# Kernel tuning notes

Hardware: AMD Instinct MI355X
Metric: run time of the kernel (lower is better)

## Reference

```python
import jax, jax.numpy as jnp
import numpy as np

B = 256
NUM_CAPS = 2            # digit capsules
N_IN = 6 * 6 * 6 * 32   # 6912 input capsules
D_OUT = 16
D_IN = 8
N_ROUTING = 3           # original loops range(3 - 1) = 2 iterations
EPS = 1e-9


def squash(s):
    # squash along last axis: (|s|^2/(1+|s|^2)) * s/|s|
    n2 = jnp.sum(s * s, axis=-1, keepdims=True)
    return (n2 / (1.0 + n2)) * s / jnp.sqrt(n2 + EPS)


def setup_inputs() -> dict:
    key = jax.random.key(0)
    k1, k2 = jax.random.split(key)
    x = jax.random.normal(k1, (B, N_IN, D_IN), dtype=jnp.float32)
    W = jax.random.normal(k2, (NUM_CAPS, N_IN, D_OUT, D_IN), dtype=jnp.float32) * 0.1
    return {"x": x, "W": W}


def reference(x, W):
    # tile x over the 2 digit capsules + per-(capsule, input-capsule) matvec:
    # u_hat[b,j,n,e] = sum_d W[j,n,e,d] * x[b,n,d]   -> [B, 2, N, 16]
    u_hat = jnp.einsum('bnd,jned->bjne', x, W)
    b_logits = jnp.zeros(u_hat.shape[:3], dtype=x.dtype)  # [B, 2, N]
    v = None
    for _ in range(N_ROUTING - 1):
        c = jax.nn.softmax(b_logits, axis=1)               # softmax over the 2 capsules (dim=1 in source)
        s = jnp.einsum('bjn,bjne->bje', c, u_hat)          # [B, 2, 16]
        v = squash(s)
        b_logits = b_logits + jnp.einsum('bje,bjne->bjn', v, u_hat)
    return v
```

## Files before the change

kernel.cpp:

```cpp
#include <hip/hip_runtime.h>

#define B_ 256
#define J_ 2
#define N_ 6912
#define E_ 16
#define D_ 8
#define NBT 18
#define CGX 384
#define TOT4 (J_*NBT*32)
#define BSTR (4*N_*D_)

__device__ __forceinline__ float dpp_row_add16(float v){
  v += __int_as_float(__builtin_amdgcn_update_dpp(0, __float_as_int(v), 0xB1,  0xF, 0xF, true));
  v += __int_as_float(__builtin_amdgcn_update_dpp(0, __float_as_int(v), 0x4E,  0xF, 0xF, true));
  v += __int_as_float(__builtin_amdgcn_update_dpp(0, __float_as_int(v), 0x141, 0xF, 0xF, true));
  v += __int_as_float(__builtin_amdgcn_update_dpp(0, __float_as_int(v), 0x140, 0xF, 0xF, true));
  return v;
}

__device__ __forceinline__ void ldx(const float* __restrict__ xp, int ni,
                                    float4 (&xa)[4], float4 (&xb)[4]){
  #pragma unroll
  for (int k=0;k<4;++k){
    xa[k] = *(const float4*)(xp + (size_t)k*BSTR + ni*8);
    xb[k] = *(const float4*)(xp + (size_t)k*BSTR + ni*8 + 4);
  }
}

__device__ __forceinline__ void body1(const float4* __restrict__ smem4, int ni,
                                      int sA, int sB,
                                      const float4 (&xa)[4], const float4 (&xb)[4],
                                      float (&acc0)[4], float (&acc1)[4]){
  const float4 wa0 = smem4[ni*32 + sA];
  const float4 wb0 = smem4[ni*32 + sB];
  const float4 wa1 = smem4[(NBT + ni)*32 + sA];
  const float4 wb1 = smem4[(NBT + ni)*32 + sB];
  #pragma unroll
  for (int k=0;k<4;++k){
    float a0 = acc0[k], a1 = acc1[k];
    a0 = fmaf(wa0.x, xa[k].x, a0); a0 = fmaf(wa0.y, xa[k].y, a0);
    a0 = fmaf(wa0.z, xa[k].z, a0); a0 = fmaf(wa0.w, xa[k].w, a0);
    a0 = fmaf(wb0.x, xb[k].x, a0); a0 = fmaf(wb0.y, xb[k].y, a0);
    a0 = fmaf(wb0.z, xb[k].z, a0); a0 = fmaf(wb0.w, xb[k].w, a0);
    a1 = fmaf(wa1.x, xa[k].x, a1); a1 = fmaf(wa1.y, xa[k].y, a1);
    a1 = fmaf(wa1.z, xa[k].z, a1); a1 = fmaf(wa1.w, xa[k].w, a1);
    a1 = fmaf(wb1.x, xb[k].x, a1); a1 = fmaf(wb1.y, xb[k].y, a1);
    a1 = fmaf(wb1.z, xb[k].z, a1); a1 = fmaf(wb1.w, xb[k].w, a1);
    acc0[k] = a0; acc1[k] = a1;
  }
}

__device__ __forceinline__ void body2(const float4* __restrict__ smem4, int ni,
                                      int sA, int sB,
                                      const float4 (&xa)[4], const float4 (&xb)[4],
                                      const float (&vj0)[4], const float (&vj1)[4],
                                      float (&acc0)[4], float (&acc1)[4]){
  const float4 wa0 = smem4[ni*32 + sA];
  const float4 wb0 = smem4[ni*32 + sB];
  const float4 wa1 = smem4[(NBT + ni)*32 + sA];
  const float4 wb1 = smem4[(NBT + ni)*32 + sB];
  float u0[4], u1[4];
  #pragma unroll
  for (int k=0;k<4;++k){
    float a0, a1;
    a0 = wa0.x*xa[k].x;            a0 = fmaf(wa0.y, xa[k].y, a0);
    a0 = fmaf(wa0.z, xa[k].z, a0); a0 = fmaf(wa0.w, xa[k].w, a0);
    a0 = fmaf(wb0.x, xb[k].x, a0); a0 = fmaf(wb0.y, xb[k].y, a0);
    a0 = fmaf(wb0.z, xb[k].z, a0); a0 = fmaf(wb0.w, xb[k].w, a0);
    a1 = wa1.x*xa[k].x;            a1 = fmaf(wa1.y, xa[k].y, a1);
    a1 = fmaf(wa1.z, xa[k].z, a1); a1 = fmaf(wa1.w, xa[k].w, a1);
    a1 = fmaf(wb1.x, xb[k].x, a1); a1 = fmaf(wb1.y, xb[k].y, a1);
    a1 = fmaf(wb1.z, xb[k].z, a1); a1 = fmaf(wb1.w, xb[k].w, a1);
    u0[k] = a0; u1[k] = a1;
  }
  #pragma unroll
  for (int k=0;k<4;++k){
    const float d  = dpp_row_add16(fmaf(vj1[k], u1[k], -(vj0[k]*u0[k])));
    const float c0 = __builtin_amdgcn_rcpf(1.f + __expf(d));
    acc0[k] = fmaf(c0,       u0[k], acc0[k]);
    acc1[k] = fmaf(1.f - c0, u1[k], acc1[k]);
  }
}

__device__ __forceinline__ void stageW(const float* __restrict__ W, int nb0, int tid,
                                       float* __restrict__ smem){
  {
    float4 buf[3];
    #pragma unroll
    for (int k=0;k<3;++k){
      const int idx = k*256 + tid;
      const int j  = (idx >= NBT*32) ? 1 : 0;
      const int r4 = idx - j*(NBT*32);
      buf[k] = *(const float4*)(W + ((size_t)j*N_ + nb0)*(E_*D_) + (size_t)r4*4);
    }
    #pragma unroll
    for (int k=0;k<3;++k){
      const int idx = k*256 + tid;
      const int u = idx & 31;
      *(float4*)(smem + (size_t)((idx & ~31) | (u ^ (u>>3)))*4) = buf[k];
    }
  }
  {
    float4 buf[2];
    #pragma unroll
    for (int k=0;k<2;++k){
      const int idx = (k+3)*256 + tid;
      if (idx < TOT4){
        const int j  = (idx >= NBT*32) ? 1 : 0;
        const int r4 = idx - j*(NBT*32);
        buf[k] = *(const float4*)(W + ((size_t)j*N_ + nb0)*(E_*D_) + (size_t)r4*4);
      }
    }
    #pragma unroll
    for (int k=0;k<2;++k){
      const int idx = (k+3)*256 + tid;
      if (idx < TOT4){
        const int u = idx & 31;
        *(float4*)(smem + (size_t)((idx & ~31) | (u ^ (u>>3)))*4) = buf[k];
      }
    }
  }
}


__global__ __launch_bounds__(256, 4) void kpass1(const float* __restrict__ x,
                                                 const float* __restrict__ W,
                                                 float* __restrict__ partial)
{
  __shared__ float smem[TOT4*4];
  const int tid  = threadIdx.x;
  const int lane = tid & 63;
  const int wv   = __builtin_amdgcn_readfirstlane(tid >> 6);
  const int e    = lane & 15;
  const int blo  = lane >> 4;
  const int nb0  = blockIdx.x * NBT;
  const int b0   = blockIdx.y*64 + wv*16 + blo;
  const float* xp = x + ((size_t)b0*N_ + nb0)*D_;
  const int sA = (e*2)   ^ ((e*2)>>3);
  const int sB = (e*2+1) ^ ((e*2+1)>>3);
  const float4* smem4 = (const float4*)smem;

  stageW(W, nb0, tid, smem);
  float4 xaA[4], xbA[4], xaB[4], xbB[4];
  ldx(xp, 0, xaA, xbA);
  __syncthreads();

  float acc0[4] = {0,0,0,0}, acc1[4] = {0,0,0,0};
  #pragma unroll 1
  for (int ni=0; ni<NBT; ni+=2){
    ldx(xp, ni+1, xaB, xbB);
    body1(smem4, ni,   sA, sB, xaA, xbA, acc0, acc1);
    if (ni+2 < NBT) ldx(xp, ni+2, xaA, xbA);
    body1(smem4, ni+1, sA, sB, xaB, xbB, acc0, acc1);
  }

  float* dst = partial + (size_t)(blockIdx.x*4 + blockIdx.y)*2048
             + (wv*16 + blo)*32 + e;
  #pragma unroll
  for (int k=0;k<4;++k){ dst[k*128] = acc0[k]; dst[k*128+16] = acc1[k]; }
}

__global__ __launch_bounds__(256, 4) void kpass2(const float* __restrict__ x,
                                                 const float* __restrict__ W,
                                                 const float* __restrict__ v1,
                                                 float* __restrict__ partial)
{
  __shared__ float smem[TOT4*4];
  const int tid  = threadIdx.x;
  const int lane = tid & 63;
  const int wv   = __builtin_amdgcn_readfirstlane(tid >> 6);
  const int e    = lane & 15;
  const int blo  = lane >> 4;
  const int nb0  = blockIdx.x * NBT;
  const int b0   = blockIdx.y*64 + wv*16 + blo;
  const float* xp = x + ((size_t)b0*N_ + nb0)*D_;
  const int sA = (e*2)   ^ ((e*2)>>3);
  const int sB = (e*2+1) ^ ((e*2+1)>>3);
  const float4* smem4 = (const float4*)smem;

  stageW(W, nb0, tid, smem);
  float4 xaA[4], xbA[4], xaB[4], xbB[4];
  ldx(xp, 0, xaA, xbA);
  float vj0[4], vj1[4];
  #pragma unroll
  for (int k=0;k<4;++k){
    vj0[k] = v1[(size_t)(b0 + 4*k)*32 + e];
    vj1[k] = v1[(size_t)(b0 + 4*k)*32 + 16 + e];
  }
  __syncthreads();

  float acc0[4] = {0,0,0,0}, acc1[4] = {0,0,0,0};
  #pragma unroll 1
  for (int ni=0; ni<NBT; ni+=2){
    ldx(xp, ni+1, xaB, xbB);
    body2(smem4, ni,   sA, sB, xaA, xbA, vj0, vj1, acc0, acc1);
    if (ni+2 < NBT) ldx(xp, ni+2, xaA, xbA);
    body2(smem4, ni+1, sA, sB, xaB, xbB, vj0, vj1, acc0, acc1);
  }

  float* dst = partial + (size_t)(blockIdx.x*4 + blockIdx.y)*2048
             + (wv*16 + blo)*32 + e;
  #pragma unroll
  for (int k=0;k<4;++k){ dst[k*128] = acc0[k]; dst[k*128+16] = acc1[k]; }
}

template<bool HALF>
__global__ __launch_bounds__(256) void kred(const float* __restrict__ partial,
                                            float* __restrict__ dst)
{
  __shared__ float sh[128];
  const int tid  = threadIdx.x;
  const int o    = blockIdx.x*128 + (tid & 127);
  const int half = tid >> 7;
  const int btile = o >> 11, q = o & 2047;
  const float* p = partial + (size_t)btile*2048 + q + (size_t)half*(CGX/2)*8192;
  float s = 0.f;
  #pragma unroll 24
  for (int cx=0; cx<CGX/2; ++cx) s += p[(size_t)cx*8192];
  if (half) sh[tid & 127] = s;
  __syncthreads();
  if (!half){
    s += sh[tid & 127];
    if (HALF) s *= 0.5f;
    float n2 = s*s;
    #pragma unroll
    for (int m=1; m<16; m<<=1) n2 += __shfl_xor(n2, m);
    dst[o] = s * (n2/(1.f+n2)) * rsqrtf(n2 + 1e-9f);
  }
}

#define NT 512
__global__ __launch_bounds__(NT) void kmono(const float* __restrict__ x,
                                            const float* __restrict__ W,
                                            float* __restrict__ out)
{
  const int b    = blockIdx.x;
  const int tid  = threadIdx.x;
  const int wv   = tid >> 6;
  const int lane = tid & 63;
  __shared__ float wred[8*33];
  __shared__ float vsh[32];

  float acc[32];
  #pragma unroll
  for (int i=0;i<32;++i) acc[i]=0.f;
  for (int n = tid; n < N_; n += NT){
    const float4 xa = *(const float4*)(x + ((size_t)b*N_ + n)*D_);
    const float4 xb = *(const float4*)(x + ((size_t)b*N_ + n)*D_ + 4);
    #pragma unroll
    for (int j=0;j<J_;++j){
      const float* wp = W + ((size_t)j*N_ + n)*(E_*D_);
      #pragma unroll
      for (int e=0;e<E_;++e){
        const float4 wa = *(const float4*)(wp + e*8);
        const float4 wb = *(const float4*)(wp + e*8 + 4);
        float a = acc[j*16+e];
        a = fmaf(wa.x,xa.x,a); a = fmaf(wa.y,xa.y,a); a = fmaf(wa.z,xa.z,a); a = fmaf(wa.w,xa.w,a);
        a = fmaf(wb.x,xb.x,a); a = fmaf(wb.y,xb.y,a); a = fmaf(wb.z,xb.z,a); a = fmaf(wb.w,xb.w,a);
        acc[j*16+e] = a;
      }
    }
  }
  #pragma unroll
  for (int i=0;i<32;++i){
    float v = acc[i];
    #pragma unroll
    for (int off=32; off; off>>=1) v += __shfl_xor(v, off);
    acc[i] = v;
  }
  if (lane == 0){
    #pragma unroll
    for (int i=0;i<32;++i) wred[wv*33 + i] = acc[i];
  }
  __syncthreads();
  if (tid < 32){
    float s = 0.f;
    #pragma unroll
    for (int w=0;w<8;++w) s += wred[w*33 + tid];
    wred[tid] = 0.5f * s;
  }
  __syncthreads();
  if (tid < 32){
    const int j = tid >> 4; float n2 = 0.f;
    #pragma unroll
    for (int e=0;e<16;++e){ const float sv = wred[j*16+e]; n2 = fmaf(sv,sv,n2); }
    vsh[tid] = wred[tid] * (n2/(1.f+n2)) * rsqrtf(n2 + 1e-9f);
  }
  __syncthreads();
  float vv[32];
  #pragma unroll
  for (int i=0;i<32;++i) vv[i] = vsh[i];

  #pragma unroll
  for (int i=0;i<32;++i) acc[i]=0.f;
  for (int n = tid; n < N_; n += NT){
    const float4 xa = *(const float4*)(x + ((size_t)b*N_ + n)*D_);
    const float4 xb = *(const float4*)(x + ((size_t)b*N_ + n)*D_ + 4);
    float u[32];
    #pragma unroll
    for (int j=0;j<J_;++j){
      const float* wp = W + ((size_t)j*N_ + n)*(E_*D_);
      #pragma unroll
      for (int e=0;e<E_;++e){
        const float4 wa = *(const float4*)(wp + e*8);
        const float4 wb = *(const float4*)(wp + e*8 + 4);
        float a;
        a = wa.x*xa.x; a = fmaf(wa.y,xa.y,a); a = fmaf(wa.z,xa.z,a); a = fmaf(wa.w,xa.w,a);
        a = fmaf(wb.x,xb.x,a); a = fmaf(wb.y,xb.y,a); a = fmaf(wb.z,xb.z,a); a = fmaf(wb.w,xb.w,a);
        u[j*16+e] = a;
      }
    }
    float l0=0.f, l1=0.f;
    #pragma unroll
    for (int e=0;e<16;++e){ l0 = fmaf(vv[e],u[e],l0); l1 = fmaf(vv[16+e],u[16+e],l1); }
    const float c0 = 1.f/(1.f + __expf(l1 - l0));
    const float c1 = 1.f - c0;
    #pragma unroll
    for (int e=0;e<16;++e){ acc[e] = fmaf(c0,u[e],acc[e]); acc[16+e] = fmaf(c1,u[16+e],acc[16+e]); }
  }
  #pragma unroll
  for (int i=0;i<32;++i){
    float v = acc[i];
    #pragma unroll
    for (int off=32; off; off>>=1) v += __shfl_xor(v, off);
    acc[i] = v;
  }
  __syncthreads();
  if (lane == 0){
    #pragma unroll
    for (int i=0;i<32;++i) wred[wv*33 + i] = acc[i];
  }
  __syncthreads();
  if (tid < 32){
    float s = 0.f;
    #pragma unroll
    for (int w=0;w<8;++w) s += wred[w*33 + tid];
    wred[tid] = s;
  }
  __syncthreads();
  if (tid < 32){
    const int j = tid >> 4; float n2 = 0.f;
    #pragma unroll
    for (int e=0;e<16;++e){ const float sv = wred[j*16+e]; n2 = fmaf(sv,sv,n2); }
    out[(size_t)b*32 + tid] = wred[tid] * (n2/(1.f+n2)) * rsqrtf(n2 + 1e-9f);
  }
}

extern "C" void kernel_launch(void* const* d_in, const int* in_sizes, int n_in,
                              void* d_out, int out_size, void* d_ws, size_t ws_size,
                              hipStream_t stream)
{
  const float* x = (const float*)d_in[0];
  const float* W = (const float*)d_in[1];
  if (n_in >= 2 && in_sizes[0] < in_sizes[1]){
    x = (const float*)d_in[1]; W = (const float*)d_in[0];
  }
  float* out = (float*)d_out;

  const size_t need = (size_t)(8192 + (size_t)CGX*4*2048) * sizeof(float);

  if (ws_size >= need){
    float* wsf     = (float*)d_ws;
    float* v1      = wsf;
    float* partial = wsf + 8192;
    kpass1<<<dim3(CGX,4), 256, 0, stream>>>(x, W, partial);
    kred<true ><<<64, 256, 0, stream>>>(partial, v1);
    kpass2<<<dim3(CGX,4), 256, 0, stream>>>(x, W, v1, partial);
    kred<false><<<64, 256, 0, stream>>>(partial, out);
  } else {
    kmono<<<B_, NT, 0, stream>>>(x, W, out);
  }
}
```

Measured before the change: 172.3 us.

## Stage x tiles through padded LDS with coalesced loads instead of per-lane register prefetch

```diff
diff --git a/kernel.cpp b/kernel.cpp
--- a/kernel.cpp
+++ b/kernel.cpp
@@ -5,10 +5,11 @@
 #define N_ 6912
 #define E_ 16
 #define D_ 8
-#define NBT 18
-#define CGX 384
+#define NBT 12
+#define CGX 576
 #define TOT4 (J_*NBT*32)
-#define BSTR (4*N_*D_)
+#define XROW 25
+#define XTOT4 (64*XROW)
 
 __device__ __forceinline__ float dpp_row_add16(float v){
   v += __int_as_float(__builtin_amdgcn_update_dpp(0, __float_as_int(v), 0xB1,  0xF, 0xF, true));
@@ -18,107 +19,36 @@
   return v;
 }
 
-__device__ __forceinline__ void ldx(const float* __restrict__ xp, int ni,
-                                    float4 (&xa)[4], float4 (&xb)[4]){
-  #pragma unroll
-  for (int k=0;k<4;++k){
-    xa[k] = *(const float4*)(xp + (size_t)k*BSTR + ni*8);
-    xb[k] = *(const float4*)(xp + (size_t)k*BSTR + ni*8 + 4);
-  }
-}
-
-__device__ __forceinline__ void body1(const float4* __restrict__ smem4, int ni,
-                                      int sA, int sB,
-                                      const float4 (&xa)[4], const float4 (&xb)[4],
-                                      float (&acc0)[4], float (&acc1)[4]){
-  const float4 wa0 = smem4[ni*32 + sA];
-  const float4 wb0 = smem4[ni*32 + sB];
-  const float4 wa1 = smem4[(NBT + ni)*32 + sA];
-  const float4 wb1 = smem4[(NBT + ni)*32 + sB];
-  #pragma unroll
-  for (int k=0;k<4;++k){
-    float a0 = acc0[k], a1 = acc1[k];
-    a0 = fmaf(wa0.x, xa[k].x, a0); a0 = fmaf(wa0.y, xa[k].y, a0);
-    a0 = fmaf(wa0.z, xa[k].z, a0); a0 = fmaf(wa0.w, xa[k].w, a0);
-    a0 = fmaf(wb0.x, xb[k].x, a0); a0 = fmaf(wb0.y, xb[k].y, a0);
-    a0 = fmaf(wb0.z, xb[k].z, a0); a0 = fmaf(wb0.w, xb[k].w, a0);
-    a1 = fmaf(wa1.x, xa[k].x, a1); a1 = fmaf(wa1.y, xa[k].y, a1);
-    a1 = fmaf(wa1.z, xa[k].z, a1); a1 = fmaf(wa1.w, xa[k].w, a1);
-    a1 = fmaf(wb1.x, xb[k].x, a1); a1 = fmaf(wb1.y, xb[k].y, a1);
-    a1 = fmaf(wb1.z, xb[k].z, a1); a1 = fmaf(wb1.w, xb[k].w, a1);
-    acc0[k] = a0; acc1[k] = a1;
-  }
-}
-
-__device__ __forceinline__ void body2(const float4* __restrict__ smem4, int ni,
-                                      int sA, int sB,
-                                      const float4 (&xa)[4], const float4 (&xb)[4],
-                                      const float (&vj0)[4], const float (&vj1)[4],
-                                      float (&acc0)[4], float (&acc1)[4]){
-  const float4 wa0 = smem4[ni*32 + sA];
-  const float4 wb0 = smem4[ni*32 + sB];
-  const float4 wa1 = smem4[(NBT + ni)*32 + sA];
-  const float4 wb1 = smem4[(NBT + ni)*32 + sB];
-  float u0[4], u1[4];
-  #pragma unroll
-  for (int k=0;k<4;++k){
-    float a0, a1;
-    a0 = wa0.x*xa[k].x;            a0 = fmaf(wa0.y, xa[k].y, a0);
-    a0 = fmaf(wa0.z, xa[k].z, a0); a0 = fmaf(wa0.w, xa[k].w, a0);
-    a0 = fmaf(wb0.x, xb[k].x, a0); a0 = fmaf(wb0.y, xb[k].y, a0);
-    a0 = fmaf(wb0.z, xb[k].z, a0); a0 = fmaf(wb0.w, xb[k].w, a0);
-    a1 = wa1.x*xa[k].x;            a1 = fmaf(wa1.y, xa[k].y, a1);
-    a1 = fmaf(wa1.z, xa[k].z, a1); a1 = fmaf(wa1.w, xa[k].w, a1);
-    a1 = fmaf(wb1.x, xb[k].x, a1); a1 = fmaf(wb1.y, xb[k].y, a1);
-    a1 = fmaf(wb1.z, xb[k].z, a1); a1 = fmaf(wb1.w, xb[k].w, a1);
-    u0[k] = a0; u1[k] = a1;
-  }
-  #pragma unroll
-  for (int k=0;k<4;++k){
-    const float d  = dpp_row_add16(fmaf(vj1[k], u1[k], -(vj0[k]*u0[k])));
-    const float c0 = __builtin_amdgcn_rcpf(1.f + __expf(d));
-    acc0[k] = fmaf(c0,       u0[k], acc0[k]);
-    acc1[k] = fmaf(1.f - c0, u1[k], acc1[k]);
-  }
-}
-
-__device__ __forceinline__ void stageW(const float* __restrict__ W, int nb0, int tid,
-                                       float* __restrict__ smem){
-  {
-    float4 buf[3];
-    #pragma unroll
-    for (int k=0;k<3;++k){
-      const int idx = k*256 + tid;
-      const int j  = (idx >= NBT*32) ? 1 : 0;
-      const int r4 = idx - j*(NBT*32);
-      buf[k] = *(const float4*)(W + ((size_t)j*N_ + nb0)*(E_*D_) + (size_t)r4*4);
-    }
-    #pragma unroll
-    for (int k=0;k<3;++k){
-      const int idx = k*256 + tid;
-      const int u = idx & 31;
-      *(float4*)(smem + (size_t)((idx & ~31) | (u ^ (u>>3)))*4) = buf[k];
-    }
-  }
-  {
-    float4 buf[2];
-    #pragma unroll
-    for (int k=0;k<2;++k){
-      const int idx = (k+3)*256 + tid;
-      if (idx < TOT4){
-        const int j  = (idx >= NBT*32) ? 1 : 0;
-        const int r4 = idx - j*(NBT*32);
-        buf[k] = *(const float4*)(W + ((size_t)j*N_ + nb0)*(E_*D_) + (size_t)r4*4);
-      }
-    }
-    #pragma unroll
-    for (int k=0;k<2;++k){
-      const int idx = (k+3)*256 + tid;
-      if (idx < TOT4){
-        const int u = idx & 31;
-        *(float4*)(smem + (size_t)((idx & ~31) | (u ^ (u>>3)))*4) = buf[k];
-      }
-    }
+__device__ __forceinline__ void stageWX(const float* __restrict__ W,
+                                        const float* __restrict__ x,
+                                        int nb0, int by64, int tid,
+                                        float4* __restrict__ Wl,
+                                        float4* __restrict__ Xl){
+  float4 bw[3], bx[6];
+  #pragma unroll
+  for (int r=0;r<3;++r){
+    const int idx = r*256 + tid;
+    const int j  = (idx >= NBT*32) ? 1 : 0;
+    const int r4 = idx - j*(NBT*32);
+    bw[r] = *(const float4*)(W + ((size_t)j*N_ + nb0)*(E_*D_) + (size_t)r4*4);
+  }
+  #pragma unroll
+  for (int r=0;r<6;++r){
+    const int g = r*256 + tid;
+    const int brow = g/24, c = g - brow*24;
+    bx[r] = *(const float4*)(x + ((size_t)(by64 + brow)*N_ + nb0)*D_ + c*4);
+  }
+  #pragma unroll
+  for (int r=0;r<3;++r){
+    const int idx = r*256 + tid;
+    const int u = idx & 31;
+    Wl[(idx & ~31) | (u ^ (u>>3))] = bw[r];
+  }
+  #pragma unroll
+  for (int r=0;r<6;++r){
+    const int g = r*256 + tid;
+    const int brow = g/24, c = g - brow*24;
+    Xl[brow*XROW + c] = bx[r];
   }
 }
 
@@ -127,7 +57,60 @@
                                                  const float* __restrict__ W,
                                                  float* __restrict__ partial)
 {
-  __shared__ float smem[TOT4*4];
+  __shared__ float4 smem4[TOT4 + XTOT4];
+  float4* Wl = smem4;
+  float4* Xl = smem4 + TOT4;
+  const int tid  = threadIdx.x;
+  const int lane = tid & 63;
+  const int wv   = __builtin_amdgcn_readfirstlane(tid >> 6);
+  const int e    = lane & 15;
+  const int blo  = lane >> 4;
+  const int nb0  = blockIdx.x * NBT;
+  const int sA = (e*2)   ^ ((e*2)>>3);
+  const int sB = (e*2+1) ^ ((e*2+1)>>3);
+
+  stageWX(W, x, nb0, blockIdx.y*64, tid, Wl, Xl);
+  __syncthreads();
+
+  const float4* Xr = Xl + (wv*16 + blo)*XROW;
+  float acc0[4] = {0,0,0,0}, acc1[4] = {0,0,0,0};
+  #pragma unroll 1
+  for (int ni=0; ni<NBT; ++ni){
+    const float4 wa0 = Wl[ni*32 + sA];
+    const float4 wb0 = Wl[ni*32 + sB];
+    const float4 wa1 = Wl[(NBT+ni)*32 + sA];
+    const float4 wb1 = Wl[(NBT+ni)*32 + sB];
+    #pragma unroll
+    for (int k=0;k<4;++k){
+      const float4 xa = Xr[k*(4*XROW) + ni*2];
+      const float4 xb = Xr[k*(4*XROW) + ni*2 + 1];
+      float a0 = acc0[k], a1 = acc1[k];
+      a0 = fmaf(wa0.x, xa.x, a0); a0 = fmaf(wa0.y, xa.y, a0);
+      a0 = fmaf(wa0.z, xa.z, a0); a0 = fmaf(wa0.w, xa.w, a0);
+      a0 = fmaf(wb0.x, xb.x, a0); a0 = fmaf(wb0.y, xb.y, a0);
+      a0 = fmaf(wb0.z, xb.z, a0); a0 = fmaf(wb0.w, xb.w, a0);
+      a1 = fmaf(wa1.x, xa.x, a1); a1 = fmaf(wa1.y, xa.y, a1);
+      a1 = fmaf(wa1.z, xa.z, a1); a1 = fmaf(wa1.w, xa.w, a1);
+      a1 = fmaf(wb1.x, xb.x, a1); a1 = fmaf(wb1.y, xb.y, a1);
+      a1 = fmaf(wb1.z, xb.z, a1); a1 = fmaf(wb1.w, xb.w, a1);
+      acc0[k] = a0; acc1[k] = a1;
+    }
+  }
+
+  float* dst = partial + (size_t)(blockIdx.x*4 + blockIdx.y)*2048
+             + (wv*16 + blo)*32 + e;
+  #pragma unroll
+  for (int k=0;k<4;++k){ dst[k*128] = acc0[k]; dst[k*128+16] = acc1[k]; }
+}
+
+__global__ __launch_bounds__(256, 4) void kpass2(const float* __restrict__ x,
+                                                 const float* __restrict__ W,
+                                                 const float* __restrict__ v1,
+                                                 float* __restrict__ partial)
+{
+  __shared__ float4 smem4[TOT4 + XTOT4];
+  float4* Wl = smem4;
+  float4* Xl = smem4 + TOT4;
   const int tid  = threadIdx.x;
   const int lane = tid & 63;
   const int wv   = __builtin_amdgcn_readfirstlane(tid >> 6);
@@ -135,52 +118,10 @@
   const int blo  = lane >> 4;
   const int nb0  = blockIdx.x * NBT;
   const int b0   = blockIdx.y*64 + wv*16 + blo;
-  const float* xp = x + ((size_t)b0*N_ + nb0)*D_;
   const int sA = (e*2)   ^ ((e*2)>>3);
   const int sB = (e*2+1) ^ ((e*2+1)>>3);
-  const float4* smem4 = (const float4*)smem;
-
-  stageW(W, nb0, tid, smem);
-  float4 xaA[4], xbA[4], xaB[4], xbB[4];
-  ldx(xp, 0, xaA, xbA);
-  __syncthreads();
-
-  float acc0[4] = {0,0,0,0}, acc1[4] = {0,0,0,0};
-  #pragma unroll 1
-  for (int ni=0; ni<NBT; ni+=2){
-    ldx(xp, ni+1, xaB, xbB);
-    body1(smem4, ni,   sA, sB, xaA, xbA, acc0, acc1);
-    if (ni+2 < NBT) ldx(xp, ni+2, xaA, xbA);
-    body1(smem4, ni+1, sA, sB, xaB, xbB, acc0, acc1);
-  }
-
-  float* dst = partial + (size_t)(blockIdx.x*4 + blockIdx.y)*2048
-             + (wv*16 + blo)*32 + e;
-  #pragma unroll
-  for (int k=0;k<4;++k){ dst[k*128] = acc0[k]; dst[k*128+16] = acc1[k]; }
-}
-
-__global__ __launch_bounds__(256, 4) void kpass2(const float* __restrict__ x,
-                                                 const float* __restrict__ W,
-                                                 const float* __restrict__ v1,
-                                                 float* __restrict__ partial)
-{
-  __shared__ float smem[TOT4*4];
-  const int tid  = threadIdx.x;
-  const int lane = tid & 63;
-  const int wv   = __builtin_amdgcn_readfirstlane(tid >> 6);
-  const int e    = lane & 15;
-  const int blo  = lane >> 4;
-  const int nb0  = blockIdx.x * NBT;
-  const int b0   = blockIdx.y*64 + wv*16 + blo;
-  const float* xp = x + ((size_t)b0*N_ + nb0)*D_;
-  const int sA = (e*2)   ^ ((e*2)>>3);
-  const int sB = (e*2+1) ^ ((e*2+1)>>3);
-  const float4* smem4 = (const float4*)smem;
-
-  stageW(W, nb0, tid, smem);
-  float4 xaA[4], xbA[4], xaB[4], xbB[4];
-  ldx(xp, 0, xaA, xbA);
+
+  stageWX(W, x, nb0, blockIdx.y*64, tid, Wl, Xl);
   float vj0[4], vj1[4];
   #pragma unroll
   for (int k=0;k<4;++k){
@@ -189,13 +130,32 @@
   }
   __syncthreads();
 
+  const float4* Xr = Xl + (wv*16 + blo)*XROW;
   float acc0[4] = {0,0,0,0}, acc1[4] = {0,0,0,0};
   #pragma unroll 1
-  for (int ni=0; ni<NBT; ni+=2){
-    ldx(xp, ni+1, xaB, xbB);
-    body2(smem4, ni,   sA, sB, xaA, xbA, vj0, vj1, acc0, acc1);
-    if (ni+2 < NBT) ldx(xp, ni+2, xaA, xbA);
-    body2(smem4, ni+1, sA, sB, xaB, xbB, vj0, vj1, acc0, acc1);
+  for (int ni=0; ni<NBT; ++ni){
+    const float4 wa0 = Wl[ni*32 + sA];
+    const float4 wb0 = Wl[ni*32 + sB];
+    const float4 wa1 = Wl[(NBT+ni)*32 + sA];
+    const float4 wb1 = Wl[(NBT+ni)*32 + sB];
+    #pragma unroll
+    for (int k=0;k<4;++k){
+      const float4 xa = Xr[k*(4*XROW) + ni*2];
+      const float4 xb = Xr[k*(4*XROW) + ni*2 + 1];
+      float a0, a1;
+      a0 = wa0.x*xa.x;          a0 = fmaf(wa0.y, xa.y, a0);
+      a0 = fmaf(wa0.z, xa.z, a0); a0 = fmaf(wa0.w, xa.w, a0);
+      a0 = fmaf(wb0.x, xb.x, a0); a0 = fmaf(wb0.y, xb.y, a0);
+      a0 = fmaf(wb0.z, xb.z, a0); a0 = fmaf(wb0.w, xb.w, a0);
+      a1 = wa1.x*xa.x;          a1 = fmaf(wa1.y, xa.y, a1);
+      a1 = fmaf(wa1.z, xa.z, a1); a1 = fmaf(wa1.w, xa.w, a1);
+      a1 = fmaf(wb1.x, xb.x, a1); a1 = fmaf(wb1.y, xb.y, a1);
+      a1 = fmaf(wb1.z, xb.z, a1); a1 = fmaf(wb1.w, xb.w, a1);
+      const float d  = dpp_row_add16(fmaf(vj1[k], a1, -(vj0[k]*a0)));
+      const float c0 = __builtin_amdgcn_rcpf(1.f + __expf(d));
+      acc0[k] = fmaf(c0,       a0, acc0[k]);
+      acc1[k] = fmaf(1.f - c0, a1, acc1[k]);
+    }
   }
 
   float* dst = partial + (size_t)(blockIdx.x*4 + blockIdx.y)*2048
```

New measurement: 153.0 us. 11.2% less time.
